# Kernel optimization log

Measured on AMD Instinct MI355X. Metric: run time of the kernel, lower is better.

## Reference

```python
import jax, jax.numpy as jnp
import numpy as np

D_MODEL = 1024
N_HEAD = 16
D_HEAD = 64


def setup_inputs() -> dict:
    key = jax.random.key(0)
    k1, k2, k3 = jax.random.split(key, 3)
    B, T = 2, 2048
    x = jax.random.normal(k1, (B, T, D_MODEL), dtype=jnp.float32)
    # Linear weights (scaled like typical init to keep softmax numerics sane)
    w_attn = jax.random.normal(k2, (D_MODEL, 3 * D_MODEL), dtype=jnp.float32) * (1.0 / np.sqrt(D_MODEL))
    w_proj = jax.random.normal(k3, (D_MODEL, D_MODEL), dtype=jnp.float32) * (1.0 / np.sqrt(D_MODEL))
    return {"x": x, "w_attn": w_attn, "w_proj": w_proj}


def reference(x, w_attn, w_proj):
    B, T, C = x.shape
    # c_attn: fused qkv projection (use_bias=False)
    qkv = jnp.einsum('btc,cf->btf', x, w_attn)  # [B, T, 3C]
    q, k, v = jnp.split(qkv, 3, axis=-1)
    q = q.reshape(B, T, N_HEAD, D_HEAD)
    k = k.reshape(B, T, N_HEAD, D_HEAD)
    v = v.reshape(B, T, N_HEAD, D_HEAD)
    # scaled QK^T with causal mask (cache=None training path)
    att = jnp.einsum('bqhd,bkhd->bhqk', q, k) * (1.0 / jnp.sqrt(jnp.float32(D_HEAD)))
    causal = jnp.tril(jnp.ones((T, T), dtype=bool))  # [T, T]
    att = jnp.where(causal[None, None, :, :], att, -jnp.inf)
    att = jax.nn.softmax(att, axis=-1)
    # dropout is a no-op (deterministic / p=0)
    y = jnp.einsum('bhqk,bkhd->bqhd', att, v).reshape(B, T, C)
    y = jnp.einsum('btc,cd->btd', y, w_proj)
    return y
```

## Files before the change

kernel.cpp:

```cpp
#include <hip/hip_runtime.h>
#include <hip/hip_bf16.h>


typedef __attribute__((ext_vector_type(8))) __bf16 bf16x8;
typedef __attribute__((ext_vector_type(4))) float  floatx4;
typedef __attribute__((ext_vector_type(4))) float  fvec4;
typedef __attribute__((ext_vector_type(4))) short  short4v;

#define MFMA16(a, b, c) __builtin_amdgcn_mfma_f32_16x16x32_bf16(a, b, c, 0, 0, 0)

using as1v = const __attribute__((address_space(1))) void;
using as3v = __attribute__((address_space(3))) void;
__device__ __forceinline__ void async16(const void* g, void* l) {
  __builtin_amdgcn_global_load_lds((as1v*)g, (as3v*)l, 16, 0, 0);
}

__device__ inline void store_out(float* p, float v) { *p = v; }
__device__ inline void store_out(__hip_bfloat16* p, float v) { *p = __float2bfloat16(v); }

__global__ __launch_bounds__(256) void prep_kernel(const float* __restrict__ x,
                                                   const float* __restrict__ w_attn,
                                                   const float* __restrict__ w_proj,
                                                   __hip_bfloat16* __restrict__ xb,
                                                   __hip_bfloat16* __restrict__ wat,
                                                   __hip_bfloat16* __restrict__ wpt) {
  const int bid = blockIdx.x, tid = threadIdx.x;
  if (bid < 4096) {
    const int i = (bid * 256 + tid) * 4;
    fvec4 v = *(const fvec4*)(x + i);
    union { short4v s; __hip_bfloat16 h[4]; } u;
#pragma unroll
    for (int j = 0; j < 4; ++j) u.h[j] = __float2bfloat16(v[j]);
    *(short4v*)((short*)xb + i) = u.s;
    return;
  }
  __shared__ __align__(16) __hip_bfloat16 tile[64 * 64];
  const float* in;
  __hip_bfloat16* out;
  int cols, bx, by;
  if (bid < 4864) {
    const int b2 = bid - 4096;
    in = w_attn; out = wat; cols = 3072; bx = b2 % 48; by = b2 / 48;
  } else {
    const int b2 = bid - 4864;
    in = w_proj; out = wpt; cols = 1024; bx = b2 % 16; by = b2 / 16;
  }
  const int c0 = bx * 64, r0 = by * 64;
#pragma unroll
  for (int it = 0; it < 2; ++it) {
    const int c = it * 256 + tid;
    const int row = c >> 3, cg = c & 7;
    const float* src = in + (long)(r0 + row) * cols + c0 + cg * 8;
    fvec4 v0 = *(const fvec4*)src;
    fvec4 v1 = *(const fvec4*)(src + 4);
    union { bf16x8 v; __hip_bfloat16 h[8]; } u;
#pragma unroll
    for (int j = 0; j < 4; ++j) { u.h[j] = __float2bfloat16(v0[j]); u.h[4 + j] = __float2bfloat16(v1[j]); }
    *(bf16x8*)(tile + row * 64 + (cg ^ ((row >> 3) & 7)) * 8) = u.v;
  }
  __syncthreads();
#pragma unroll
  for (int it = 0; it < 2; ++it) {
    const int c = it * 256 + tid;
    const int dr = c >> 3, tg = c & 7;
    union { bf16x8 v; __hip_bfloat16 e[8]; } u;
    const int pg = (dr >> 3) ^ tg;
#pragma unroll
    for (int j = 0; j < 8; ++j)
      u.e[j] = tile[(tg * 8 + j) * 64 + pg * 8 + (dr & 7)];
    *(bf16x8*)(out + (long)(c0 + dr) * 1024 + r0 + tg * 8) = u.v;
  }
}

__global__ __launch_bounds__(256) void gemm_qkv_kernel(const __hip_bfloat16* __restrict__ A,
                                                       const __hip_bfloat16* __restrict__ Bt,
                                                       __hip_bfloat16* __restrict__ qk,
                                                       __hip_bfloat16* __restrict__ vt,
                                                       float qscale) {
  const int K = 1024;
  __shared__ __align__(16) __hip_bfloat16 As[2][128 * 32];
  __shared__ __align__(16) __hip_bfloat16 Bs[2][128 * 32];
  const int tid = threadIdx.x;
  const int lane = tid & 63, wv = tid >> 6;
  const int l15 = lane & 15, quad = lane >> 4;
  const int wm = wv >> 1, wn = wv & 1;
  const long m0 = (long)blockIdx.y * 128, n0 = (long)blockIdx.x * 128;
  floatx4 acc[4][4] = {};
  const int nk = K >> 5;

  auto issue = [&](int kt, int p) {
    const int k0 = kt << 5;
#pragma unroll
    for (int it = 0; it < 2; ++it) {
      const int c = it * 256 + tid;
      const int row = c >> 2;
      const int lcg = (c & 3) ^ ((row >> 1) & 3);
      async16(A + (m0 + row) * K + k0 + lcg * 8, (char*)&As[p][0] + c * 16);
      async16(Bt + (n0 + row) * K + k0 + lcg * 8, (char*)&Bs[p][0] + c * 16);
    }
  };

  issue(0, 0);
  for (int kt = 0; kt < nk; ++kt) {
    const int p = kt & 1;
    __syncthreads();
    if (kt + 1 < nk) issue(kt + 1, p ^ 1);
    bf16x8 af[4], bfr[4];
#pragma unroll
    for (int t = 0; t < 4; ++t) {
      const int ar = wm * 64 + t * 16 + l15;
      const int br = wn * 64 + t * 16 + l15;
      af[t]  = *(const bf16x8*)(&As[p][ar * 32 + (quad ^ ((ar >> 1) & 3)) * 8]);
      bfr[t] = *(const bf16x8*)(&Bs[p][br * 32 + (quad ^ ((br >> 1) & 3)) * 8]);
    }
#pragma unroll
    for (int mt = 0; mt < 4; ++mt)
#pragma unroll
      for (int nt = 0; nt < 4; ++nt)
        acc[mt][nt] = MFMA16(af[mt], bfr[nt], acc[mt][nt]);
  }

#pragma unroll
  for (int nt = 0; nt < 4; ++nt) {
    const int colb = (int)n0 + wn * 64 + nt * 16;
    if (colb >= 2048) {
      const int hh = (colb - 2048) >> 6;
      const int d  = (colb & 63) + l15;
#pragma unroll
      for (int mt = 0; mt < 4; ++mt) {
        const long row = m0 + wm * 64 + mt * 16 + quad * 4;
        const long b   = row >> 11;
        const long t0  = row & 2047;
        union { short4v s; __hip_bfloat16 h[4]; } uy;
#pragma unroll
        for (int r = 0; r < 4; ++r) uy.h[r] = __float2bfloat16(acc[mt][nt][r]);
        *(short4v*)(vt + ((b * 16 + hh) * 64 + d) * 2048 + t0) = uy.s;
      }
    } else {
      const float sc = (colb < 1024) ? qscale : 1.0f;
      const long col = colb + l15;
#pragma unroll
      for (int mt = 0; mt < 4; ++mt)
#pragma unroll
        for (int r = 0; r < 4; ++r) {
          const long row = m0 + wm * 64 + mt * 16 + quad * 4 + r;
          qk[row * 2048 + col] = __float2bfloat16(acc[mt][nt][r] * sc);
        }
    }
  }
}

template <typename OutT>
__global__ __launch_bounds__(256) void gemm_bt64_kernel(const __hip_bfloat16* __restrict__ A,
                                                        const __hip_bfloat16* __restrict__ Bt,
                                                        OutT* __restrict__ C,
                                                        int M, int N, int K) {
  __shared__ __align__(16) __hip_bfloat16 As[2][128 * 32];
  __shared__ __align__(16) __hip_bfloat16 Bs[2][64 * 32];
  const int tid = threadIdx.x;
  const int lane = tid & 63, wv = tid >> 6;
  const int l15 = lane & 15, quad = lane >> 4;
  const int wm = wv >> 1, wn = wv & 1;
  const long m0 = (long)blockIdx.y * 128, n0 = (long)blockIdx.x * 64;
  floatx4 acc[4][2] = {};
  const int nk = K >> 5;

  auto issue = [&](int kt, int p) {
    const int k0 = kt << 5;
#pragma unroll
    for (int it = 0; it < 2; ++it) {
      const int c = it * 256 + tid;
      const int row = c >> 2;
      const int lcg = (c & 3) ^ ((row >> 1) & 3);
      async16(A + (m0 + row) * K + k0 + lcg * 8, (char*)&As[p][0] + c * 16);
    }
    {
      const int c = tid;
      const int row = c >> 2;
      const int lcg = (c & 3) ^ ((row >> 1) & 3);
      async16(Bt + (n0 + row) * K + k0 + lcg * 8, (char*)&Bs[p][0] + c * 16);
    }
  };

  issue(0, 0);
  for (int kt = 0; kt < nk; ++kt) {
    const int p = kt & 1;
    __syncthreads();
    if (kt + 1 < nk) issue(kt + 1, p ^ 1);
    bf16x8 af[4], bfr[2];
#pragma unroll
    for (int t = 0; t < 4; ++t) {
      const int ar = wm * 64 + t * 16 + l15;
      af[t] = *(const bf16x8*)(&As[p][ar * 32 + (quad ^ ((ar >> 1) & 3)) * 8]);
    }
#pragma unroll
    for (int t = 0; t < 2; ++t) {
      const int br = wn * 32 + t * 16 + l15;
      bfr[t] = *(const bf16x8*)(&Bs[p][br * 32 + (quad ^ ((br >> 1) & 3)) * 8]);
    }
#pragma unroll
    for (int mt = 0; mt < 4; ++mt)
#pragma unroll
      for (int nt = 0; nt < 2; ++nt)
        acc[mt][nt] = MFMA16(af[mt], bfr[nt], acc[mt][nt]);
  }
#pragma unroll
  for (int mt = 0; mt < 4; ++mt)
#pragma unroll
    for (int nt = 0; nt < 2; ++nt)
#pragma unroll
      for (int r = 0; r < 4; ++r) {
        const long row = m0 + wm * 64 + mt * 16 + quad * 4 + r;
        const long col = n0 + wn * 32 + nt * 16 + l15;
        store_out(C + row * N + col, acc[mt][nt][r]);
      }
}

__global__ __launch_bounds__(256) void attn_kernel(const __hip_bfloat16* __restrict__ qk,
                                                   const __hip_bfloat16* __restrict__ vtg,
                                                   __hip_bfloat16* __restrict__ y) {
  __shared__ __align__(16) __hip_bfloat16 Ks[2][64 * 64];
  __shared__ __align__(16) __hip_bfloat16 Vt[2][64 * 64];
  __shared__ __align__(16) __hip_bfloat16 Pb[4][16 * 64];
  const int tid = threadIdx.x;
  const int lane = tid & 63, wv = tid >> 6;
  const int l15 = lane & 15, quad = lane >> 4;
  const int pt = blockIdx.x, h = blockIdx.y, b = blockIdx.z;
  const int qtA = pt, qtB = 31 - pt;
  const int q0A = qtA * 64, q0B = qtB * 64;
  const long bh = (long)b * 16 + h;
  const long RS = 2048;

  auto issue = [&](int kt, int p) {
    const int kb = kt * 64;
#pragma unroll
    for (int it = 0; it < 2; ++it) {
      const int c = it * 256 + tid;
      const int row = c >> 3;
      const int cg = (c & 7) ^ (row & 7);
      async16(qk + ((long)b * 2048 + kb + row) * RS + 1024 + h * 64 + cg * 8,
              (char*)&Ks[p][0] + c * 16);
      async16(vtg + (bh * 64 + row) * 2048 + kb + cg * 8, (char*)&Vt[p][0] + c * 16);
    }
  };

  bf16x8 bqA0, bqA1, bqB0, bqB1;
  {
    const __hip_bfloat16* qpA = qk + ((long)b * 2048 + q0A + wv * 16 + l15) * RS + h * 64 + quad * 8;
    bqA0 = *(const bf16x8*)qpA;
    bqA1 = *(const bf16x8*)(qpA + 32);
    const __hip_bfloat16* qpB = qk + ((long)b * 2048 + q0B + wv * 16 + l15) * RS + h * 64 + quad * 8;
    bqB0 = *(const bf16x8*)qpB;
    bqB1 = *(const bf16x8*)(qpB + 32);
  }
  union { bf16x8 v; __hip_bfloat16 e[8]; } uo;
#pragma unroll
  for (int j = 0; j < 8; ++j) uo.e[j] = __float2bfloat16(1.0f);
  const bf16x8 ones = uo.v;

  floatx4 oA[4] = {}, oB[4] = {}, o4A = {}, o4B = {};
  __hip_bfloat16* Pw = &Pb[wv][0];
  const int m7 = l15 & 7;

  issue(0, 0);
  for (int kt = 0; kt <= qtB; ++kt) {
    const int p = kt & 1;
    const int kb = kt * 64;
    const bool actA = (kt <= qtA);
    __syncthreads();
    if (kt < qtB) issue(kt + 1, p ^ 1);

    bf16x8 kf[4][2], vf[4][2];
#pragma unroll
    for (int nt = 0; nt < 4; ++nt) {
      const int row = nt * 16 + l15;
      const int s0 = (quad ^ (row & 7)) * 8, s1 = ((quad + 4) ^ (row & 7)) * 8;
      kf[nt][0] = *(const bf16x8*)(&Ks[p][row * 64 + s0]);
      kf[nt][1] = *(const bf16x8*)(&Ks[p][row * 64 + s1]);
      vf[nt][0] = *(const bf16x8*)(&Vt[p][row * 64 + s0]);
      vf[nt][1] = *(const bf16x8*)(&Vt[p][row * 64 + s1]);
    }

    auto tile = [&](const bf16x8& bq0, const bf16x8& bq1, floatx4* o, floatx4& o4,
                    bool diag, int q0X) {
      floatx4 st[4] = {};
#pragma unroll
      for (int nt = 0; nt < 4; ++nt) {
        st[nt] = MFMA16(kf[nt][0], bq0, st[nt]);
        st[nt] = MFMA16(kf[nt][1], bq1, st[nt]);
      }
      const int qg = q0X + wv * 16 + l15;
#pragma unroll
      for (int nt = 0; nt < 4; ++nt) {
        union { short4v s; __hip_bfloat16 h[4]; } up;
#pragma unroll
        for (int r = 0; r < 4; ++r) {
          float pv = exp2f(st[nt][r]);
          if (diag && (kb + nt * 16 + quad * 4 + r > qg)) pv = 0.f;
          up.h[r] = __float2bfloat16(pv);
        }
        const int chunk = (nt * 2 + (quad >> 1)) ^ m7;
        *(short4v*)(Pw + l15 * 64 + chunk * 8 + (quad & 1) * 4) = up.s;
      }
      const bf16x8 pb0 = *(const bf16x8*)(Pw + l15 * 64 + (quad ^ m7) * 8);
      const bf16x8 pb1 = *(const bf16x8*)(Pw + l15 * 64 + ((quad + 4) ^ m7) * 8);
#pragma unroll
      for (int mt = 0; mt < 4; ++mt) {
        o[mt] = MFMA16(vf[mt][0], pb0, o[mt]);
        o[mt] = MFMA16(vf[mt][1], pb1, o[mt]);
      }
      o4 = MFMA16(ones, pb0, o4);
      o4 = MFMA16(ones, pb1, o4);
    };

    tile(bqB0, bqB1, oB, o4B, kt == qtB, q0B);
    if (actA) tile(bqA0, bqA1, oA, o4A, kt == qtA, q0A);
  }

  auto epi = [&](floatx4* o, floatx4& o4, int q0X) {
    const float inv = 1.0f / o4[0];
    const long t = (long)b * 2048 + q0X + wv * 16 + l15;
#pragma unroll
    for (int mt = 0; mt < 4; ++mt) {
      union { short4v s; __hip_bfloat16 h[4]; } uy;
#pragma unroll
      for (int r = 0; r < 4; ++r) uy.h[r] = __float2bfloat16(o[mt][r] * inv);
      *(short4v*)(y + t * 1024 + h * 64 + mt * 16 + quad * 4) = uy.s;
    }
  };
  epi(oA, o4A, q0A);
  epi(oB, o4B, q0B);
}

extern "C" void kernel_launch(void* const* d_in, const int* in_sizes, int n_in,
                              void* d_out, int out_size, void* d_ws, size_t ws_size,
                              hipStream_t stream) {
  const float* x      = (const float*)d_in[0];
  const float* w_attn = (const float*)d_in[1];
  const float* w_proj = (const float*)d_in[2];
  float* out = (float*)d_out;
  char* ws = (char*)d_ws;
  __hip_bfloat16* xb  = (__hip_bfloat16*)(ws);
  __hip_bfloat16* wat = (__hip_bfloat16*)(ws + 8388608);
  __hip_bfloat16* qk  = (__hip_bfloat16*)(ws + 16777216);
  __hip_bfloat16* wpt = (__hip_bfloat16*)(ws + 33554432);
  __hip_bfloat16* vtg = (__hip_bfloat16*)(ws + 35651584);
  __hip_bfloat16* yb  = wat;
  const float SC = 0.18033688011112042f;

  prep_kernel<<<5120, 256, 0, stream>>>(x, w_attn, w_proj, xb, wat, wpt);
  gemm_qkv_kernel<<<dim3(24, 32), 256, 0, stream>>>(xb, wat, qk, vtg, SC);
  attn_kernel<<<dim3(16, 16, 2), 256, 0, stream>>>(qk, vtg, yb);
  gemm_bt64_kernel<float><<<dim3(16, 32), 256, 0, stream>>>(yb, wpt, out, 4096, 1024, 1024);
}
```

Before: 183.3 us.

## Split attention KV loop across two wave groups with LDS reduction

The attention block grows from 256 to 512 threads. Two groups of four waves each process alternating 64-key tiles, loaded two at a time into double-buffered LDS, and their partial outputs and row sums are combined through shared memory before the epilogue. The causal-mask check is also split out so non-diagonal tiles skip the per-element comparison. This doubles the waves working on each query pair and halves the serial length of the key loop, at the cost of more LDS (80KB), an extra reduction step and possible idle waves when the tile count is odd.

```diff
diff --git a/kernel.cpp b/kernel.cpp
--- a/kernel.cpp
+++ b/kernel.cpp
@@ -216,40 +216,48 @@
       }
 }
 
-__global__ __launch_bounds__(256) void attn_kernel(const __hip_bfloat16* __restrict__ qk,
-                                                   const __hip_bfloat16* __restrict__ vtg,
-                                                   __hip_bfloat16* __restrict__ y) {
-  __shared__ __align__(16) __hip_bfloat16 Ks[2][64 * 64];
-  __shared__ __align__(16) __hip_bfloat16 Vt[2][64 * 64];
-  __shared__ __align__(16) __hip_bfloat16 Pb[4][16 * 64];
+__global__ __launch_bounds__(512, 4) void attn_kernel(const __hip_bfloat16* __restrict__ qk,
+                                                      const __hip_bfloat16* __restrict__ vtg,
+                                                      __hip_bfloat16* __restrict__ y) {
+  __shared__ __align__(16) char smem[81920];
+  __hip_bfloat16* KsB = (__hip_bfloat16*)smem;
+  __hip_bfloat16* VtB = (__hip_bfloat16*)(smem + 32768);
+  __hip_bfloat16* PbB = (__hip_bfloat16*)(smem + 65536);
+
   const int tid = threadIdx.x;
   const int lane = tid & 63, wv = tid >> 6;
   const int l15 = lane & 15, quad = lane >> 4;
+  const int g = wv >> 2, sub = wv & 3;
   const int pt = blockIdx.x, h = blockIdx.y, b = blockIdx.z;
   const int qtA = pt, qtB = 31 - pt;
   const int q0A = qtA * 64, q0B = qtB * 64;
   const long bh = (long)b * 16 + h;
   const long RS = 2048;
 
-  auto issue = [&](int kt, int p) {
-    const int kb = kt * 64;
-#pragma unroll
-    for (int it = 0; it < 2; ++it) {
-      const int c = it * 256 + tid;
-      const int row = c >> 3;
-      const int cg = (c & 7) ^ (row & 7);
-      async16(qk + ((long)b * 2048 + kb + row) * RS + 1024 + h * 64 + cg * 8,
-              (char*)&Ks[p][0] + c * 16);
-      async16(vtg + (bh * 64 + row) * 2048 + kb + cg * 8, (char*)&Vt[p][0] + c * 16);
+  const int srow = tid >> 3;
+  const int scg = (tid & 7) ^ (srow & 7);
+  const __hip_bfloat16* kbase = qk + ((long)b * 2048 + srow) * RS + 1024 + h * 64 + scg * 8;
+  const __hip_bfloat16* vbase = vtg + (bh * 64 + srow) * 2048 + scg * 8;
+  char* ldst = smem + tid * 16;
+
+  auto issue = [&](int pr, int buf) {
+#pragma unroll
+    for (int par = 0; par < 2; ++par) {
+      const int kt = 2 * pr + par;
+      if (kt <= qtB) {
+        const long kb = (long)kt * 64;
+        async16(kbase + kb * RS, ldst + buf * 16384 + par * 8192);
+        async16(vbase + kb,      ldst + 32768 + buf * 16384 + par * 8192);
+      }
     }
   };
 
   bf16x8 bqA0, bqA1, bqB0, bqB1;
   {
-    const __hip_bfloat16* qpA = qk + ((long)b * 2048 + q0A + wv * 16 + l15) * RS + h * 64 + quad * 8;
+    const __hip_bfloat16* qpA = qk + ((long)b * 2048 + q0A + sub * 16 + l15) * RS + h * 64 + quad * 8;
     bqA0 = *(const bf16x8*)qpA;
     bqA1 = *(const bf16x8*)(qpA + 32);
-    const __hip_bfloat16* qpB = qk + ((long)b * 2048 + q0B + wv * 16 + l15) * RS + h * 64 + quad * 8;
+    const __hip_bfloat16* qpB = qk + ((long)b * 2048 + q0B + sub * 16 + l15) * RS + h * 64 + quad * 8;
     bqB0 = *(const bf16x8*)qpB;
     bqB1 = *(const bf16x8*)(qpB + 32);
   }
@@ -259,26 +267,30 @@
   const bf16x8 ones = uo.v;
 
   floatx4 oA[4] = {}, oB[4] = {}, o4A = {}, o4B = {};
-  __hip_bfloat16* Pw = &Pb[wv][0];
+  __hip_bfloat16* Pw = PbB + wv * (16 * 64);
   const int m7 = l15 & 7;
 
+  const int npairs = (qtB + 2) >> 1;
   issue(0, 0);
-  for (int kt = 0; kt <= qtB; ++kt) {
-    const int p = kt & 1;
+  for (int pr = 0; pr < npairs; ++pr) {
+    const int buf = pr & 1;
+    __syncthreads();
+    if (pr + 1 < npairs) issue(pr + 1, buf ^ 1);
+    const int kt = 2 * pr + g;
+    if (kt > qtB) continue;
     const int kb = kt * 64;
-    const bool actA = (kt <= qtA);
-    __syncthreads();
-    if (kt < qtB) issue(kt + 1, p ^ 1);
+    const __hip_bfloat16* Ksp = KsB + buf * 8192 + g * 4096;
+    const __hip_bfloat16* Vsp = VtB + buf * 8192 + g * 4096;
 
     bf16x8 kf[4][2], vf[4][2];
 #pragma unroll
     for (int nt = 0; nt < 4; ++nt) {
       const int row = nt * 16 + l15;
       const int s0 = (quad ^ (row & 7)) * 8, s1 = ((quad + 4) ^ (row & 7)) * 8;
-      kf[nt][0] = *(const bf16x8*)(&Ks[p][row * 64 + s0]);
-      kf[nt][1] = *(const bf16x8*)(&Ks[p][row * 64 + s1]);
-      vf[nt][0] = *(const bf16x8*)(&Vt[p][row * 64 + s0]);
-      vf[nt][1] = *(const bf16x8*)(&Vt[p][row * 64 + s1]);
+      kf[nt][0] = *(const bf16x8*)(Ksp + row * 64 + s0);
+      kf[nt][1] = *(const bf16x8*)(Ksp + row * 64 + s1);
+      vf[nt][0] = *(const bf16x8*)(Vsp + row * 64 + s0);
+      vf[nt][1] = *(const bf16x8*)(Vsp + row * 64 + s1);
     }
 
     auto tile = [&](const bf16x8& bq0, const bf16x8& bq1, floatx4* o, floatx4& o4,
@@ -289,18 +301,29 @@
         st[nt] = MFMA16(kf[nt][0], bq0, st[nt]);
         st[nt] = MFMA16(kf[nt][1], bq1, st[nt]);
       }
-      const int qg = q0X + wv * 16 + l15;
-#pragma unroll
-      for (int nt = 0; nt < 4; ++nt) {
-        union { short4v s; __hip_bfloat16 h[4]; } up;
-#pragma unroll
-        for (int r = 0; r < 4; ++r) {
-          float pv = exp2f(st[nt][r]);
-          if (diag && (kb + nt * 16 + quad * 4 + r > qg)) pv = 0.f;
-          up.h[r] = __float2bfloat16(pv);
+      if (diag) {
+        const int qg = q0X + sub * 16 + l15;
+#pragma unroll
+        for (int nt = 0; nt < 4; ++nt) {
+          union { short4v s; __hip_bfloat16 h[4]; } up;
+#pragma unroll
+          for (int r = 0; r < 4; ++r) {
+            float pv = exp2f(st[nt][r]);
+            if (kb + nt * 16 + quad * 4 + r > qg) pv = 0.f;
+            up.h[r] = __float2bfloat16(pv);
+          }
+          const int chunk = (nt * 2 + (quad >> 1)) ^ m7;
+          *(short4v*)(Pw + l15 * 64 + chunk * 8 + (quad & 1) * 4) = up.s;
         }
-        const int chunk = (nt * 2 + (quad >> 1)) ^ m7;
-        *(short4v*)(Pw + l15 * 64 + chunk * 8 + (quad & 1) * 4) = up.s;
+      } else {
+#pragma unroll
+        for (int nt = 0; nt < 4; ++nt) {
+          union { short4v s; __hip_bfloat16 h[4]; } up;
+#pragma unroll
+          for (int r = 0; r < 4; ++r) up.h[r] = __float2bfloat16(exp2f(st[nt][r]));
+          const int chunk = (nt * 2 + (quad >> 1)) ^ m7;
+          *(short4v*)(Pw + l15 * 64 + chunk * 8 + (quad & 1) * 4) = up.s;
+        }
       }
       const bf16x8 pb0 = *(const bf16x8*)(Pw + l15 * 64 + (quad ^ m7) * 8);
       const bf16x8 pb1 = *(const bf16x8*)(Pw + l15 * 64 + ((quad + 4) ^ m7) * 8);
@@ -314,22 +337,44 @@
     };
 
     tile(bqB0, bqB1, oB, o4B, kt == qtB, q0B);
-    if (actA) tile(bqA0, bqA1, oA, o4A, kt == qtA, q0A);
-  }
-
-  auto epi = [&](floatx4* o, floatx4& o4, int q0X) {
-    const float inv = 1.0f / o4[0];
-    const long t = (long)b * 2048 + q0X + wv * 16 + l15;
+    if (kt <= qtA) tile(bqA0, bqA1, oA, o4A, kt == qtA, q0A);
+  }
+
+  __syncthreads();
+  floatx4* redv = (floatx4*)smem;
+  if (g == 1) {
 #pragma unroll
     for (int mt = 0; mt < 4; ++mt) {
-      union { short4v s; __hip_bfloat16 h[4]; } uy;
-#pragma unroll
-      for (int r = 0; r < 4; ++r) uy.h[r] = __float2bfloat16(o[mt][r] * inv);
-      *(short4v*)(y + t * 1024 + h * 64 + mt * 16 + quad * 4) = uy.s;
-    }
-  };
-  epi(oA, o4A, q0A);
-  epi(oB, o4B, q0B);
+      redv[(sub * 10 + mt) * 64 + lane] = oA[mt];
+      redv[(sub * 10 + 4 + mt) * 64 + lane] = oB[mt];
+    }
+    redv[(sub * 10 + 8) * 64 + lane] = o4A;
+    redv[(sub * 10 + 9) * 64 + lane] = o4B;
+  }
+  __syncthreads();
+  if (g == 0) {
+#pragma unroll
+    for (int mt = 0; mt < 4; ++mt) {
+      oA[mt] += redv[(sub * 10 + mt) * 64 + lane];
+      oB[mt] += redv[(sub * 10 + 4 + mt) * 64 + lane];
+    }
+    o4A += redv[(sub * 10 + 8) * 64 + lane];
+    o4B += redv[(sub * 10 + 9) * 64 + lane];
+
+    auto epi = [&](floatx4* o, floatx4& o4, int q0X) {
+      const float inv = 1.0f / o4[0];
+      const long t = (long)b * 2048 + q0X + sub * 16 + l15;
+#pragma unroll
+      for (int mt = 0; mt < 4; ++mt) {
+        union { short4v s; __hip_bfloat16 h[4]; } uy;
+#pragma unroll
+        for (int r = 0; r < 4; ++r) uy.h[r] = __float2bfloat16(o[mt][r] * inv);
+        *(short4v*)(y + t * 1024 + h * 64 + mt * 16 + quad * 4) = uy.s;
+      }
+    };
+    epi(oA, o4A, q0A);
+    epi(oB, o4B, q0B);
+  }
 }
 
 extern "C" void kernel_launch(void* const* d_in, const int* in_sizes, int n_in,
@@ -350,6 +395,6 @@
 
   prep_kernel<<<5120, 256, 0, stream>>>(x, w_attn, w_proj, xb, wat, wpt);
   gemm_qkv_kernel<<<dim3(24, 32), 256, 0, stream>>>(xb, wat, qk, vtg, SC);
-  attn_kernel<<<dim3(16, 16, 2), 256, 0, stream>>>(qk, vtg, yb);
+  attn_kernel<<<dim3(16, 16, 2), 512, 0, stream>>>(qk, vtg, yb);
   gemm_bt64_kernel<float><<<dim3(16, 32), 256, 0, stream>>>(yb, wpt, out, 4096, 1024, 1024);
 }
```

After: 245.8 us. +34.1%, slower.

## Split attention key loop across two blocks with atomic fp32 accumulation and merge

Applied to the files above, without the earlier changes.

Each attention work item is now split between two blocks, one handling even key tiles and one handling odd key tiles, which doubles the grid. Each block atomically adds its unnormalized output and softmax denominator into zeroed fp32 buffers. A new merge kernel then normalizes and converts the result to bf16 for the projection GEMM. This raises parallelism and occupancy in the attention kernel. In exchange it adds two memsets, many global atomics, an extra 16MB round trip and one more launch.

```diff
diff --git a/kernel.cpp b/kernel.cpp
--- a/kernel.cpp
+++ b/kernel.cpp
@@ -218,14 +218,16 @@
 
 __global__ __launch_bounds__(256) void attn_kernel(const __hip_bfloat16* __restrict__ qk,
                                                    const __hip_bfloat16* __restrict__ vtg,
-                                                   __hip_bfloat16* __restrict__ y) {
+                                                   float* __restrict__ oacc,
+                                                   float* __restrict__ dacc) {
   __shared__ __align__(16) __hip_bfloat16 Ks[2][64 * 64];
   __shared__ __align__(16) __hip_bfloat16 Vt[2][64 * 64];
   __shared__ __align__(16) __hip_bfloat16 Pb[4][16 * 64];
   const int tid = threadIdx.x;
   const int lane = tid & 63, wv = tid >> 6;
   const int l15 = lane & 15, quad = lane >> 4;
-  const int pt = blockIdx.x, h = blockIdx.y, b = blockIdx.z;
+  const int pt = blockIdx.x >> 1, par = blockIdx.x & 1;
+  const int h = blockIdx.y, b = blockIdx.z;
   const int qtA = pt, qtB = 31 - pt;
   const int q0A = qtA * 64, q0B = qtB * 64;
   const long bh = (long)b * 16 + h;
@@ -262,23 +264,23 @@
   __hip_bfloat16* Pw = &Pb[wv][0];
   const int m7 = l15 & 7;
 
-  issue(0, 0);
-  for (int kt = 0; kt <= qtB; ++kt) {
-    const int p = kt & 1;
+  issue(par, 0);
+  int bufp = 0;
+  for (int kt = par; kt <= qtB; kt += 2, bufp ^= 1) {
     const int kb = kt * 64;
     const bool actA = (kt <= qtA);
     __syncthreads();
-    if (kt < qtB) issue(kt + 1, p ^ 1);
+    if (kt + 2 <= qtB) issue(kt + 2, bufp ^ 1);
 
     bf16x8 kf[4][2], vf[4][2];
 #pragma unroll
     for (int nt = 0; nt < 4; ++nt) {
       const int row = nt * 16 + l15;
       const int s0 = (quad ^ (row & 7)) * 8, s1 = ((quad + 4) ^ (row & 7)) * 8;
-      kf[nt][0] = *(const bf16x8*)(&Ks[p][row * 64 + s0]);
-      kf[nt][1] = *(const bf16x8*)(&Ks[p][row * 64 + s1]);
-      vf[nt][0] = *(const bf16x8*)(&Vt[p][row * 64 + s0]);
-      vf[nt][1] = *(const bf16x8*)(&Vt[p][row * 64 + s1]);
+      kf[nt][0] = *(const bf16x8*)(&Ks[bufp][row * 64 + s0]);
+      kf[nt][1] = *(const bf16x8*)(&Ks[bufp][row * 64 + s1]);
+      vf[nt][0] = *(const bf16x8*)(&Vt[bufp][row * 64 + s0]);
+      vf[nt][1] = *(const bf16x8*)(&Vt[bufp][row * 64 + s1]);
     }
 
     auto tile = [&](const bf16x8& bq0, const bf16x8& bq1, floatx4* o, floatx4& o4,
@@ -318,18 +320,30 @@
   }
 
   auto epi = [&](floatx4* o, floatx4& o4, int q0X) {
-    const float inv = 1.0f / o4[0];
     const long t = (long)b * 2048 + q0X + wv * 16 + l15;
-#pragma unroll
-    for (int mt = 0; mt < 4; ++mt) {
-      union { short4v s; __hip_bfloat16 h[4]; } uy;
-#pragma unroll
-      for (int r = 0; r < 4; ++r) uy.h[r] = __float2bfloat16(o[mt][r] * inv);
-      *(short4v*)(y + t * 1024 + h * 64 + mt * 16 + quad * 4) = uy.s;
-    }
+    float* ob = oacc + t * 1024 + h * 64 + quad * 4;
+#pragma unroll
+    for (int mt = 0; mt < 4; ++mt)
+#pragma unroll
+      for (int r = 0; r < 4; ++r)
+        atomicAdd(ob + mt * 16 + r, o[mt][r]);
+    if (quad == 0) atomicAdd(dacc + t * 16 + h, o4[0]);
   };
   epi(oA, o4A, q0A);
   epi(oB, o4B, q0B);
+}
+
+__global__ __launch_bounds__(256) void merge_kernel(const float* __restrict__ oacc,
+                                                    const float* __restrict__ dacc,
+                                                    __hip_bfloat16* __restrict__ y) {
+  const int i = (blockIdx.x * 256 + threadIdx.x) * 4;
+  const int row = i >> 10, hh = (i >> 6) & 15;
+  const float inv = 1.0f / dacc[row * 16 + hh];
+  fvec4 v = *(const fvec4*)(oacc + i);
+  union { short4v s; __hip_bfloat16 h[4]; } u;
+#pragma unroll
+  for (int j = 0; j < 4; ++j) u.h[j] = __float2bfloat16(v[j] * inv);
+  *(short4v*)((short*)y + i) = u.s;
 }
 
 extern "C" void kernel_launch(void* const* d_in, const int* in_sizes, int n_in,
@@ -345,11 +359,16 @@
   __hip_bfloat16* qk  = (__hip_bfloat16*)(ws + 16777216);
   __hip_bfloat16* wpt = (__hip_bfloat16*)(ws + 33554432);
   __hip_bfloat16* vtg = (__hip_bfloat16*)(ws + 35651584);
-  __hip_bfloat16* yb  = wat;
+  float* oacc = (float*)ws;
+  float* dacc = (float*)out;
+  __hip_bfloat16* yb = vtg;
   const float SC = 0.18033688011112042f;
 
   prep_kernel<<<5120, 256, 0, stream>>>(x, w_attn, w_proj, xb, wat, wpt);
   gemm_qkv_kernel<<<dim3(24, 32), 256, 0, stream>>>(xb, wat, qk, vtg, SC);
-  attn_kernel<<<dim3(16, 16, 2), 256, 0, stream>>>(qk, vtg, yb);
+  hipMemsetAsync(ws, 0, 16777216, stream);
+  hipMemsetAsync(out, 0, 262144, stream);
+  attn_kernel<<<dim3(32, 16, 2), 256, 0, stream>>>(qk, vtg, oacc, dacc);
+  merge_kernel<<<4096, 256, 0, stream>>>(oacc, dacc, yb);
   gemm_bt64_kernel<float><<<dim3(16, 32), 256, 0, stream>>>(yb, wpt, out, 4096, 1024, 1024);
 }
```

After: 288.0 us. 1.57x slower.
